# Performance work log

Hardware: AMD Instinct MI355X
Metric: run time of the kernel (lower is better)

The kernel has to match this reference:

```python
import jax, jax.numpy as jnp
import numpy as np

DIM = 1024
HEADS = 16
DIM_HEAD = 64
INNER = HEADS * DIM_HEAD  # 1024
SCALE = DIM_HEAD ** -0.5


def setup_inputs() -> dict:
    key = jax.random.key(0)
    k0, k1, k2 = jax.random.split(key, 3)
    x = jax.random.normal(k0, (4, 2048, DIM), dtype=jnp.float32)
    ln_gamma = jnp.ones((DIM,), dtype=jnp.float32)
    ln_beta = jnp.zeros((DIM,), dtype=jnp.float32)
    w_qkv = jax.random.normal(k1, (DIM, 3 * INNER), dtype=jnp.float32) * (DIM ** -0.5)
    w_out = jax.random.normal(k2, (INNER, DIM), dtype=jnp.float32) * (INNER ** -0.5)
    b_out = jnp.zeros((DIM,), dtype=jnp.float32)
    return {"x": x, "ln_gamma": ln_gamma, "ln_beta": ln_beta,
            "w_qkv": w_qkv, "w_out": w_out, "b_out": b_out}


def reference(x, ln_gamma, ln_beta, w_qkv, w_out, b_out):
    # LayerNorm over last dim (eps matches torch default 1e-5)
    mu = jnp.mean(x, axis=-1, keepdims=True)
    var = jnp.mean(jnp.square(x - mu), axis=-1, keepdims=True)
    xn = (x - mu) * jax.lax.rsqrt(var + 1e-5) * ln_gamma + ln_beta
    # QKV projection (no bias)
    qkv = xn @ w_qkv  # [b, t, 3*inner]
    q, k, v = jnp.split(qkv, 3, axis=-1)
    B, T, _ = x.shape
    def to_heads(t):
        return t.reshape(B, T, HEADS, DIM_HEAD).transpose(0, 2, 1, 3)  # b h t d
    q, k, v = to_heads(q), to_heads(k), to_heads(v)
    dots = jnp.einsum('bhid,bhjd->bhij', q, k) * SCALE
    attn = jax.nn.softmax(dots, axis=-1)
    out = jnp.einsum('bhij,bhjd->bhid', attn, v)
    out = out.transpose(0, 2, 1, 3).reshape(B, T, INNER)
    return out @ w_out + b_out
```

## Files before the change

### kernel.cpp

```cpp
#include <hip/hip_runtime.h>


#define DIMX 1024
#define TSEQ 2048
#define NB 4
#define NH 16
#define DH 64
#define NROWS (NB * TSEQ)
#define QSCALE 0.18033688011112042f

typedef __bf16 bf16_t;
typedef __bf16 bf16x8 __attribute__((ext_vector_type(8)));
typedef __bf16 bf16x4 __attribute__((ext_vector_type(4)));
typedef float f32x4 __attribute__((ext_vector_type(4)));

#if __has_builtin(__builtin_amdgcn_exp2f)
#define EXP2F __builtin_amdgcn_exp2f
#else
#define EXP2F exp2f
#endif

__device__ __forceinline__ bf16x4 cvt4(f32x4 v) {
    return __builtin_convertvector(v, bf16x4);
}
__device__ __forceinline__ void async16(const bf16_t* g, bf16_t* l) {
    __builtin_amdgcn_global_load_lds(
        (const __attribute__((address_space(1))) unsigned int*)g,
        (__attribute__((address_space(3))) unsigned int*)l, 16, 0, 0);
}

__global__ __launch_bounds__(256) void prep_kernel(
    const float* __restrict__ x, const float* __restrict__ g,
    const float* __restrict__ b, bf16_t* __restrict__ xn,
    const float* __restrict__ w_qkv, bf16_t* __restrict__ wqkvT,
    const float* __restrict__ w_out, bf16_t* __restrict__ woutT) {
    int bid = blockIdx.x, tid = threadIdx.x;
    if (bid < NROWS) {
        int row = bid;
        const float4 xv = *(const float4*)(x + (size_t)row * DIMX + tid * 4);
        float s = xv.x + xv.y + xv.z + xv.w;
        float q = xv.x * xv.x + xv.y * xv.y + xv.z * xv.z + xv.w * xv.w;
        for (int o = 32; o > 0; o >>= 1) {
            s += __shfl_xor(s, o);
            q += __shfl_xor(q, o);
        }
        __shared__ float2 red[4];
        int wave = tid >> 6, lane = tid & 63;
        if (lane == 0) red[wave] = make_float2(s, q);
        __syncthreads();
        float2 r0 = red[0], r1 = red[1], r2 = red[2], r3 = red[3];
        s = r0.x + r1.x + r2.x + r3.x;
        q = r0.y + r1.y + r2.y + r3.y;
        float mu = s * (1.0f / DIMX);
        float var = q * (1.0f / DIMX) - mu * mu;
        float rstd = rsqrtf(var + 1e-5f);
        float4 gv = *(const float4*)(g + tid * 4);
        float4 bv = *(const float4*)(b + tid * 4);
        f32x4 r;
        r[0] = (xv.x - mu) * rstd * gv.x + bv.x;
        r[1] = (xv.y - mu) * rstd * gv.y + bv.y;
        r[2] = (xv.z - mu) * rstd * gv.z + bv.z;
        r[3] = (xv.w - mu) * rstd * gv.w + bv.w;
        *(bf16x4*)(xn + (size_t)row * DIMX + tid * 4) = cvt4(r);
    } else {
        const float* src;
        bf16_t* dst;
        int R, C, tb;
        if (bid < NROWS + 3072) {
            tb = bid - NROWS; src = w_qkv; dst = wqkvT; R = 1024; C = 3072;
        } else {
            tb = bid - NROWS - 3072; src = w_out; dst = woutT; R = 1024; C = 1024;
        }
        int ntx = C >> 5;
        int c0 = (tb % ntx) * 32, r0 = (tb / ntx) * 32;
        int tx = tid & 31, ty = tid >> 5;
        __shared__ float tile[32][33];
        for (int i = ty; i < 32; i += 8)
            tile[i][tx] = src[(size_t)(r0 + i) * C + c0 + tx];
        __syncthreads();
        for (int i = ty; i < 32; i += 8)
            dst[(size_t)(c0 + i) * R + r0 + tx] = (bf16_t)tile[tx][i];
    }
}

#define MFMA16 __builtin_amdgcn_mfma_f32_16x16x32_bf16

template <int MODE>
__device__ __forceinline__ void gemm_epilogue(
    f32x4 (&acc)[4][4], void* Cout, const float* bias,
    int m0, int n0, int wr, int wc, int lm, int quad, int N) {
#pragma unroll
    for (int mt = 0; mt < 4; ++mt) {
#pragma unroll
        for (int nt = 0; nt < 4; ++nt) {
            int m = m0 + wr * 64 + mt * 16 + quad * 4;
            int n = n0 + wc * 64 + nt * 16 + lm;
            if (MODE == 1) {
                int sel = n >> 10, nn = n & 1023, h = nn >> 6, d = nn & 63;
                int b = m >> 11, t = m & 2047;
                if (sel == 2) {
                    *(bf16x4*)((bf16_t*)Cout + (size_t)2 * 8388608 +
                               ((size_t)((b * NH + h) * DH + d)) * TSEQ + t) = cvt4(acc[mt][nt]);
                } else {
                    f32x4 sv = acc[mt][nt] * (sel == 0 ? QSCALE : 1.0f);
                    bf16x4 c4 = cvt4(sv);
#pragma unroll
                    for (int r = 0; r < 4; ++r)
                        ((bf16_t*)Cout)[(size_t)sel * 8388608 +
                                        ((size_t)((b * NH + h) * TSEQ + t + r)) * DH + d] = c4[r];
                }
            } else {
                float bn = bias[n];
#pragma unroll
                for (int r = 0; r < 4; ++r)
                    ((float*)Cout)[(size_t)(m + r) * N + n] = acc[mt][nt][r] + bn;
            }
        }
    }
}

template <int MODE>
__global__ __launch_bounds__(256, 2) void gemm128p(
    const bf16_t* __restrict__ A, const bf16_t* __restrict__ BT,
    void* __restrict__ Cout, const float* __restrict__ bias, int M, int N, int K) {
    __shared__ __align__(16) bf16_t As[2][128 * 64];
    __shared__ __align__(16) bf16_t Bs[2][128 * 64];
    int tid = threadIdx.x, lane = tid & 63, wave = tid >> 6;
    int lm = lane & 15, quad = lane >> 4;
    int wr = wave >> 1, wc = wave & 1;

    int nbx = gridDim.x;
    int nwg = nbx * gridDim.y;
    int linear = blockIdx.y * nbx + blockIdx.x;
    int cpx = nwg >> 3;
    int swz = (linear & 7) * cpx + (linear >> 3);
    int bx = swz % nbx, by = swz / nbx;
    int m0 = by * 128, n0 = bx * 128;

    int srow = tid >> 3, sc8 = tid & 7;
    int scol = (sc8 ^ (srow & 7)) << 3;
    const bf16_t* ga = A + (size_t)(m0 + srow) * K + scol;
    const bf16_t* gb = BT + (size_t)(n0 + srow) * K + scol;
    int ldst = tid << 3;

    int sw0 = ((quad ^ (lm & 7)) << 3);
    int sw1 = (((4 + quad) ^ (lm & 7)) << 3);

    f32x4 zero = {0.f, 0.f, 0.f, 0.f};
    f32x4 acc[4][4];
#pragma unroll
    for (int i = 0; i < 4; ++i)
#pragma unroll
        for (int j = 0; j < 4; ++j) acc[i][j] = zero;

#pragma unroll
    for (int i = 0; i < 4; ++i) async16(ga + (size_t)(i * 32) * K, &As[0][i * 2048 + ldst]);
#pragma unroll
    for (int i = 0; i < 4; ++i) async16(gb + (size_t)(i * 32) * K, &Bs[0][i * 2048 + ldst]);
    asm volatile("s_waitcnt vmcnt(0)" ::: "memory");
    __builtin_amdgcn_s_barrier();

    int nkt = K >> 6;
    for (int kt = 0; kt < nkt; ++kt) {
        int c = kt & 1;
        int k1 = (kt + 1) << 6;
        bool pf = (kt + 1) < nkt;
        const bf16_t* pa = &As[c][0];
        const bf16_t* pb = &Bs[c][0];
        bf16_t* na = &As[c ^ 1][0];
        bf16_t* nb = &Bs[c ^ 1][0];
        bf16x8 af[4][2], bfr[2][2];

#pragma unroll
        for (int t = 0; t < 4; ++t) {
            int ro = (wr * 64 + t * 16 + lm) * 64;
            af[t][0] = *(const bf16x8*)&pa[ro + sw0];
            af[t][1] = *(const bf16x8*)&pa[ro + sw1];
        }
#pragma unroll
        for (int t = 0; t < 2; ++t) {
            int ro = (wc * 64 + t * 16 + lm) * 64;
            bfr[t][0] = *(const bf16x8*)&pb[ro + sw0];
            bfr[t][1] = *(const bf16x8*)&pb[ro + sw1];
        }
        if (pf) {
#pragma unroll
            for (int i = 0; i < 4; ++i)
                async16(ga + (size_t)(i * 32) * K + k1, &na[i * 2048 + ldst]);
#pragma unroll
            for (int i = 0; i < 4; ++i)
                async16(gb + (size_t)(i * 32) * K + k1, &nb[i * 2048 + ldst]);
        }
        __builtin_amdgcn_s_barrier();
        asm volatile("s_waitcnt lgkmcnt(0)" ::: "memory");
        __builtin_amdgcn_s_setprio(1);
#pragma unroll
        for (int mt = 0; mt < 4; ++mt)
#pragma unroll
            for (int nt = 0; nt < 2; ++nt) {
                acc[mt][nt] = MFMA16(af[mt][0], bfr[nt][0], acc[mt][nt], 0, 0, 0);
                acc[mt][nt] = MFMA16(af[mt][1], bfr[nt][1], acc[mt][nt], 0, 0, 0);
            }
        __builtin_amdgcn_s_setprio(0);
        __builtin_amdgcn_s_barrier();

#pragma unroll
        for (int t = 0; t < 2; ++t) {
            int ro = (wc * 64 + (2 + t) * 16 + lm) * 64;
            bfr[t][0] = *(const bf16x8*)&pb[ro + sw0];
            bfr[t][1] = *(const bf16x8*)&pb[ro + sw1];
        }
        __builtin_amdgcn_s_barrier();
        asm volatile("s_waitcnt lgkmcnt(0)" ::: "memory");
        __builtin_amdgcn_s_setprio(1);
#pragma unroll
        for (int mt = 0; mt < 4; ++mt)
#pragma unroll
            for (int nt = 0; nt < 2; ++nt) {
                acc[mt][2 + nt] = MFMA16(af[mt][0], bfr[nt][0], acc[mt][2 + nt], 0, 0, 0);
                acc[mt][2 + nt] = MFMA16(af[mt][1], bfr[nt][1], acc[mt][2 + nt], 0, 0, 0);
            }
        __builtin_amdgcn_s_setprio(0);
        asm volatile("s_waitcnt vmcnt(0)" ::: "memory");
        __builtin_amdgcn_s_barrier();
    }

    gemm_epilogue<MODE>(acc, Cout, bias, m0, n0, wr, wc, lm, quad, N);
}

__global__ __launch_bounds__(512, 4) void attn_mfma(
    const bf16_t* __restrict__ qkv, bf16_t* __restrict__ o) {
    int bh = blockIdx.y;
    int qt = blockIdx.x;
    const bf16_t* qb = qkv + (size_t)bh * TSEQ * DH;
    const bf16_t* kb = qkv + (size_t)8388608 + (size_t)bh * TSEQ * DH;
    const bf16_t* vb = qkv + (size_t)16777216 + (size_t)bh * DH * TSEQ;
    int tid = threadIdx.x, wave = tid >> 6, lane = tid & 63;
    int lm = lane & 15, quad = lane >> 4, lx = lm & 7;

    __shared__ __align__(16) bf16_t Ks[2][2][64 * 64];
    __shared__ __align__(16) bf16_t Vt[2][2][64 * 64];

    int roff = tid >> 3;
    int fr = (roff & 3) | ((roff & 8) >> 1);
    int cperm = ((tid & 7) ^ fr) * 8;
    const bf16_t* kp = kb + (size_t)roff * DH + cperm;
    const bf16_t* vp = vb + (size_t)roff * TSEQ + cperm;
    int l0 = tid * 8;

    bf16x8 qf[2][2];
#pragma unroll
    for (int u = 0; u < 2; ++u)
#pragma unroll
        for (int ks = 0; ks < 2; ++ks)
            qf[u][ks] = *(const bf16x8*)(qb +
                (size_t)(qt * 256 + wave * 32 + u * 16 + lm) * DH + ks * 32 + quad * 8);

    f32x4 zero = {0.f, 0.f, 0.f, 0.f};
    f32x4 m16 = {-16.f, -16.f, -16.f, -16.f};
    f32x4 acc[2][4];
#pragma unroll
    for (int u = 0; u < 2; ++u)
#pragma unroll
        for (int dt = 0; dt < 4; ++dt) acc[u][dt] = zero;
    f32x4 l4[2] = {zero, zero};

    int qh = lm >> 2, rr = lm & 3;
    int krow0 = 8 * qh + rr;
    int krow1 = krow0 + 4;
    int krow2 = 32 + 8 * (qh ^ 2) + rr;
    int krow3 = krow2 + 4;
    int fo0 = (quad ^ lx) * 8;
    int fo1 = ((4 + quad) ^ lx) * 8;
    int fv = (lm & 3) | ((lm & 8) >> 1);
    int vo0 = (quad ^ fv) * 8;
    int vo1 = ((4 | (quad ^ 2)) ^ fv) * 8;

    async16(kp, &Ks[0][0][l0]);
    async16(kp + (size_t)64 * DH, &Ks[0][1][l0]);
    async16(vp, &Vt[0][0][l0]);
    async16(vp + 64, &Vt[0][1][l0]);
    kp += 128 * DH; vp += 128;
    asm volatile("s_waitcnt vmcnt(0)" ::: "memory");
    __builtin_amdgcn_s_barrier();

    for (int jt = 0; jt < TSEQ / 128; ++jt) {
        int c = jt & 1;
        if (jt + 1 < TSEQ / 128) {
            async16(kp, &Ks[c ^ 1][0][l0]);
            async16(kp + (size_t)64 * DH, &Ks[c ^ 1][1][l0]);
            async16(vp, &Vt[c ^ 1][0][l0]);
            async16(vp + 64, &Vt[c ^ 1][1][l0]);
            kp += 128 * DH; vp += 128;
        }

#pragma unroll
        for (int sub = 0; sub < 2; ++sub) {
            const bf16_t* Kc = &Ks[c][sub][0];
            const bf16_t* Vc = &Vt[c][sub][0];

            bf16x8 kf[4][2];
            kf[0][0] = *(const bf16x8*)&Kc[krow0 * 64 + fo0];
            kf[0][1] = *(const bf16x8*)&Kc[krow0 * 64 + fo1];
            kf[1][0] = *(const bf16x8*)&Kc[krow1 * 64 + fo0];
            kf[1][1] = *(const bf16x8*)&Kc[krow1 * 64 + fo1];
            kf[2][0] = *(const bf16x8*)&Kc[krow2 * 64 + fo0];
            kf[2][1] = *(const bf16x8*)&Kc[krow2 * 64 + fo1];
            kf[3][0] = *(const bf16x8*)&Kc[krow3 * 64 + fo0];
            kf[3][1] = *(const bf16x8*)&Kc[krow3 * 64 + fo1];

            f32x4 s2[2][4];
            __builtin_amdgcn_s_setprio(1);
#pragma unroll
            for (int u = 0; u < 2; ++u)
#pragma unroll
                for (int nt = 0; nt < 4; ++nt) {
                    s2[u][nt] = __builtin_amdgcn_mfma_f32_16x16x32_bf16(kf[nt][0], qf[u][0], m16, 0, 0, 0);
                    s2[u][nt] = __builtin_amdgcn_mfma_f32_16x16x32_bf16(kf[nt][1], qf[u][1], s2[u][nt], 0, 0, 0);
                }
            __builtin_amdgcn_s_setprio(0);

            bf16x8 pf[2][2];
#pragma unroll
            for (int u = 0; u < 2; ++u) {
                f32x4 p[4];
#pragma unroll
                for (int nt = 0; nt < 4; ++nt) {
#pragma unroll
                    for (int e = 0; e < 4; ++e) p[nt][e] = EXP2F(s2[u][nt][e]);
                    l4[u] += p[nt];
                }
                bf16x4 c0 = cvt4(p[0]), c1 = cvt4(p[1]), c2 = cvt4(p[2]), c3 = cvt4(p[3]);
                pf[u][0] = __builtin_shufflevector(c0, c1, 0, 1, 2, 3, 4, 5, 6, 7);
                pf[u][1] = __builtin_shufflevector(c2, c3, 0, 1, 2, 3, 4, 5, 6, 7);
            }

            __builtin_amdgcn_s_setprio(1);
#pragma unroll
            for (int dt = 0; dt < 4; ++dt) {
                bf16x8 vf0 = *(const bf16x8*)&Vc[(dt * 16 + lm) * 64 + vo0];
                bf16x8 vf1 = *(const bf16x8*)&Vc[(dt * 16 + lm) * 64 + vo1];
#pragma unroll
                for (int u = 0; u < 2; ++u) {
                    acc[u][dt] = __builtin_amdgcn_mfma_f32_16x16x32_bf16(vf0, pf[u][0], acc[u][dt], 0, 0, 0);
                    acc[u][dt] = __builtin_amdgcn_mfma_f32_16x16x32_bf16(vf1, pf[u][1], acc[u][dt], 0, 0, 0);
                }
            }
            __builtin_amdgcn_s_setprio(0);
        }

        asm volatile("s_waitcnt vmcnt(0)" ::: "memory");
        __builtin_amdgcn_s_barrier();
    }

    int b = bh >> 4, h = bh & 15;
#pragma unroll
    for (int u = 0; u < 2; ++u) {
        float l = (l4[u][0] + l4[u][1]) + (l4[u][2] + l4[u][3]);
        l += __shfl_xor(l, 16);
        l += __shfl_xor(l, 32);
        float rl = 1.0f / l;
        int t = qt * 256 + wave * 32 + u * 16 + lm;
#pragma unroll
        for (int dt = 0; dt < 4; ++dt) {
            f32x4 ov = acc[u][dt] * rl;
            *(bf16x4*)(o + ((size_t)(b * TSEQ + t)) * DIMX + h * DH + dt * 16 + quad * 4) = cvt4(ov);
        }
    }
}

extern "C" void kernel_launch(void* const* d_in, const int* in_sizes, int n_in,
                              void* d_out, int out_size, void* d_ws, size_t ws_size,
                              hipStream_t stream) {
    const float* x = (const float*)d_in[0];
    const float* g = (const float*)d_in[1];
    const float* be = (const float*)d_in[2];
    const float* w_qkv = (const float*)d_in[3];
    const float* w_out = (const float*)d_in[4];
    const float* b_out = (const float*)d_in[5];
    float* out = (float*)d_out;
    char* ws = (char*)d_ws;

    bf16_t* xn = (bf16_t*)(ws);
    bf16_t* wqkvT = (bf16_t*)(ws + 16777216);
    bf16_t* woutT = (bf16_t*)(ws + 23068672);
    bf16_t* qkv = (bf16_t*)(ws + 25165824);
    bf16_t* attno = (bf16_t*)(ws + 75497472);

    prep_kernel<<<NROWS + 3072 + 1024, 256, 0, stream>>>(
        x, g, be, xn, w_qkv, wqkvT, w_out, woutT);
    gemm128p<1><<<dim3(24, 64), 256, 0, stream>>>(xn, wqkvT, (void*)qkv, nullptr, NROWS, 3072, 1024);
    attn_mfma<<<dim3(8, 64), 512, 0, stream>>>(qkv, attno);
    gemm128p<2><<<dim3(8, 64), 256, 0, stream>>>(attno, woutT, (void*)out, b_out, NROWS, 1024, 1024);
}
```

Before: 258.4 us.

## Use 256x256-tile 8-wave GEMM kernel for QKV projection

Adds a new GEMM kernel with 256x256 output tiles, 512 threads and 8 waves, each wave computing a 128x64 sub-tile. A and B halves are staged asynchronously into double-buffered LDS, and the loads are interleaved with four MFMA phases per K-step. The larger tile is meant to cut global and LDS traffic per FLOP for the QKV projection. In exchange it uses more registers and 128KB of LDS, limiting occupancy to one block per CU, and the grid shrinks to 384 blocks, which may leave the 256 CUs unevenly loaded.

```diff
diff --git a/kernel.cpp b/kernel.cpp
--- a/kernel.cpp
+++ b/kernel.cpp
@@ -86,37 +86,190 @@
 #define MFMA16 __builtin_amdgcn_mfma_f32_16x16x32_bf16
 
 template <int MODE>
-__device__ __forceinline__ void gemm_epilogue(
-    f32x4 (&acc)[4][4], void* Cout, const float* bias,
-    int m0, int n0, int wr, int wc, int lm, int quad, int N) {
-#pragma unroll
-    for (int mt = 0; mt < 4; ++mt) {
+__device__ __forceinline__ void cwrite_frag(
+    f32x4 v, void* Cout, const float* bias, int m, int n, int N) {
+    if (MODE == 1) {
+        int sel = n >> 10, nn = n & 1023, h = nn >> 6, d = nn & 63;
+        int b = m >> 11, t = m & 2047;
+        if (sel == 2) {
+            *(bf16x4*)((bf16_t*)Cout + (size_t)2 * 8388608 +
+                       ((size_t)((b * NH + h) * DH + d)) * TSEQ + t) = cvt4(v);
+        } else {
+            f32x4 sv = v * (sel == 0 ? QSCALE : 1.0f);
+            bf16x4 c4 = cvt4(sv);
+#pragma unroll
+            for (int r = 0; r < 4; ++r)
+                ((bf16_t*)Cout)[(size_t)sel * 8388608 +
+                                ((size_t)((b * NH + h) * TSEQ + t + r)) * DH + d] = c4[r];
+        }
+    } else {
+        float bn = bias[n];
+#pragma unroll
+        for (int r = 0; r < 4; ++r)
+            ((float*)Cout)[(size_t)(m + r) * N + n] = v[r] + bn;
+    }
+}
+
+template <int MODE>
+__global__ __launch_bounds__(512, 1) void gemm256t(
+    const bf16_t* __restrict__ A, const bf16_t* __restrict__ BT,
+    void* __restrict__ Cout, const float* __restrict__ bias, int M, int N, int K) {
+    __shared__ __align__(16) bf16_t Ah[2][2][128 * 64];
+    __shared__ __align__(16) bf16_t Bh[2][2][128 * 64];
+    int tid = threadIdx.x, lane = tid & 63, wave = tid >> 6;
+    int lm = lane & 15, quad = lane >> 4;
+    int wr = wave >> 2, wc = wave & 3;
+
+    int nbx = gridDim.x;
+    int nwg = nbx * gridDim.y;
+    int linear = blockIdx.y * nbx + blockIdx.x;
+    int cpx = nwg >> 3;
+    int swz = (linear & 7) * cpx + (linear >> 3);
+    int bx = swz % nbx, by = swz / nbx;
+    int m0 = by * 256, n0 = bx * 256;
+
+    int srow = tid >> 3;
+    int scol = ((tid & 7) ^ (srow & 7)) << 3;
+    const bf16_t* ga = A + (size_t)(m0 + srow) * K + scol;
+    const bf16_t* gb = BT + (size_t)(n0 + srow) * K + scol;
+    int ldst = tid * 8;
+
+#define STAGE_A(t, H)                                                          \
+    do {                                                                       \
+        size_t k0 = (size_t)(t) << 6;                                          \
+        async16(ga + (size_t)((H) * 128) * K + k0, &Ah[(t)&1][H][ldst]);       \
+        async16(ga + (size_t)((H) * 128 + 64) * K + k0,                        \
+                &Ah[(t)&1][H][4096 + ldst]);                                   \
+    } while (0)
+#define STAGE_B(t, H)                                                          \
+    do {                                                                       \
+        size_t k0 = (size_t)(t) << 6;                                          \
+        async16(gb + (size_t)((H) * 128) * K + k0, &Bh[(t)&1][H][ldst]);       \
+        async16(gb + (size_t)((H) * 128 + 64) * K + k0,                        \
+                &Bh[(t)&1][H][4096 + ldst]);                                   \
+    } while (0)
+
+    int sw0 = ((quad ^ (lm & 7)) << 3);
+    int sw1 = (((4 + quad) ^ (lm & 7)) << 3);
+    int brow = (wc & 1) * 64;
+
+    f32x4 zero = {0.f, 0.f, 0.f, 0.f};
+    f32x4 acc[8][4];
+#pragma unroll
+    for (int i = 0; i < 8; ++i)
+#pragma unroll
+        for (int j = 0; j < 4; ++j) acc[i][j] = zero;
+
+    STAGE_A(0, 0);
+    STAGE_A(0, 1);
+    STAGE_B(0, 0);
+    STAGE_B(0, 1);
+    STAGE_A(1, 0);
+    STAGE_A(1, 1);
+
+    int nkt = K >> 6;
+    bf16x8 af[4][2], bfa[2][2], bfb[2][2];
+    for (int t = 0; t < nkt; ++t) {
+        int s = t & 1;
+        const bf16_t* pA = &Ah[s][wr][0];
+        const bf16_t* pB = &Bh[s][wc >> 1][0];
+
+        if (t + 1 < nkt) STAGE_B(t + 1, 0);
+        if (t < nkt - 1)
+            asm volatile("s_waitcnt vmcnt(6)" ::: "memory");
+        else
+            asm volatile("s_waitcnt vmcnt(0)" ::: "memory");
+        __builtin_amdgcn_s_barrier();
+#pragma unroll
+        for (int mt = 0; mt < 4; ++mt) {
+            int ro = (mt * 16 + lm) * 64;
+            af[mt][0] = *(const bf16x8*)&pA[ro + sw0];
+            af[mt][1] = *(const bf16x8*)&pA[ro + sw1];
+        }
+#pragma unroll
+        for (int nt = 0; nt < 2; ++nt) {
+            int ro = (brow + nt * 16 + lm) * 64;
+            bfa[nt][0] = *(const bf16x8*)&pB[ro + sw0];
+            bfa[nt][1] = *(const bf16x8*)&pB[ro + sw1];
+        }
+        asm volatile("s_waitcnt lgkmcnt(0)" ::: "memory");
+        __builtin_amdgcn_s_setprio(1);
+#pragma unroll
+        for (int mt = 0; mt < 4; ++mt)
+#pragma unroll
+            for (int nt = 0; nt < 2; ++nt) {
+                acc[mt][nt] = MFMA16(af[mt][0], bfa[nt][0], acc[mt][nt], 0, 0, 0);
+                acc[mt][nt] = MFMA16(af[mt][1], bfa[nt][1], acc[mt][nt], 0, 0, 0);
+            }
+        __builtin_amdgcn_s_setprio(0);
+        __builtin_amdgcn_s_barrier();
+
+#pragma unroll
+        for (int nt = 0; nt < 2; ++nt) {
+            int ro = (brow + (2 + nt) * 16 + lm) * 64;
+            bfb[nt][0] = *(const bf16x8*)&pB[ro + sw0];
+            bfb[nt][1] = *(const bf16x8*)&pB[ro + sw1];
+        }
+        if (t + 1 < nkt) STAGE_B(t + 1, 1);
+        __builtin_amdgcn_s_barrier();
+        asm volatile("s_waitcnt lgkmcnt(0)" ::: "memory");
+        __builtin_amdgcn_s_setprio(1);
+#pragma unroll
+        for (int mt = 0; mt < 4; ++mt)
+#pragma unroll
+            for (int nt = 0; nt < 2; ++nt) {
+                acc[mt][2 + nt] = MFMA16(af[mt][0], bfb[nt][0], acc[mt][2 + nt], 0, 0, 0);
+                acc[mt][2 + nt] = MFMA16(af[mt][1], bfb[nt][1], acc[mt][2 + nt], 0, 0, 0);
+            }
+        __builtin_amdgcn_s_setprio(0);
+        __builtin_amdgcn_s_barrier();
+
+#pragma unroll
+        for (int mt = 0; mt < 4; ++mt) {
+            int ro = (64 + mt * 16 + lm) * 64;
+            af[mt][0] = *(const bf16x8*)&pA[ro + sw0];
+            af[mt][1] = *(const bf16x8*)&pA[ro + sw1];
+        }
+        __builtin_amdgcn_s_barrier();
+        asm volatile("s_waitcnt lgkmcnt(0)" ::: "memory");
+        __builtin_amdgcn_s_setprio(1);
+#pragma unroll
+        for (int mt = 0; mt < 4; ++mt)
+#pragma unroll
+            for (int nt = 0; nt < 2; ++nt) {
+                acc[4 + mt][2 + nt] = MFMA16(af[mt][0], bfb[nt][0], acc[4 + mt][2 + nt], 0, 0, 0);
+                acc[4 + mt][2 + nt] = MFMA16(af[mt][1], bfb[nt][1], acc[4 + mt][2 + nt], 0, 0, 0);
+            }
+        __builtin_amdgcn_s_setprio(0);
+        __builtin_amdgcn_s_barrier();
+
+        if (t + 2 < nkt) {
+            STAGE_A(t + 2, 0);
+            STAGE_A(t + 2, 1);
+        }
+        __builtin_amdgcn_s_barrier();
+        __builtin_amdgcn_s_setprio(1);
+#pragma unroll
+        for (int mt = 0; mt < 4; ++mt)
+#pragma unroll
+            for (int nt = 0; nt < 2; ++nt) {
+                acc[4 + mt][nt] = MFMA16(af[mt][0], bfa[nt][0], acc[4 + mt][nt], 0, 0, 0);
+                acc[4 + mt][nt] = MFMA16(af[mt][1], bfa[nt][1], acc[4 + mt][nt], 0, 0, 0);
+            }
+        __builtin_amdgcn_s_setprio(0);
+        __builtin_amdgcn_s_barrier();
+    }
+#undef STAGE_A
+#undef STAGE_B
+
+#pragma unroll
+    for (int mt = 0; mt < 8; ++mt)
 #pragma unroll
         for (int nt = 0; nt < 4; ++nt) {
-            int m = m0 + wr * 64 + mt * 16 + quad * 4;
+            int m = m0 + wr * 128 + mt * 16 + quad * 4;
             int n = n0 + wc * 64 + nt * 16 + lm;
-            if (MODE == 1) {
-                int sel = n >> 10, nn = n & 1023, h = nn >> 6, d = nn & 63;
-                int b = m >> 11, t = m & 2047;
-                if (sel == 2) {
-                    *(bf16x4*)((bf16_t*)Cout + (size_t)2 * 8388608 +
-                               ((size_t)((b * NH + h) * DH + d)) * TSEQ + t) = cvt4(acc[mt][nt]);
-                } else {
-                    f32x4 sv = acc[mt][nt] * (sel == 0 ? QSCALE : 1.0f);
-                    bf16x4 c4 = cvt4(sv);
-#pragma unroll
-                    for (int r = 0; r < 4; ++r)
-                        ((bf16_t*)Cout)[(size_t)sel * 8388608 +
-                                        ((size_t)((b * NH + h) * TSEQ + t + r)) * DH + d] = c4[r];
-                }
-            } else {
-                float bn = bias[n];
-#pragma unroll
-                for (int r = 0; r < 4; ++r)
-                    ((float*)Cout)[(size_t)(m + r) * N + n] = acc[mt][nt][r] + bn;
-            }
-        }
-    }
+            cwrite_frag<MODE>(acc[mt][nt], Cout, bias, m, n, N);
+        }
 }
 
 template <int MODE>
@@ -225,7 +378,14 @@
         __builtin_amdgcn_s_barrier();
     }
 
-    gemm_epilogue<MODE>(acc, Cout, bias, m0, n0, wr, wc, lm, quad, N);
+#pragma unroll
+    for (int mt = 0; mt < 4; ++mt)
+#pragma unroll
+        for (int nt = 0; nt < 4; ++nt) {
+            int m = m0 + wr * 64 + mt * 16 + quad * 4;
+            int n = n0 + wc * 64 + nt * 16 + lm;
+            cwrite_frag<MODE>(acc[mt][nt], Cout, bias, m, n, N);
+        }
 }
 
 __global__ __launch_bounds__(512, 4) void attn_mfma(
@@ -389,7 +549,7 @@
 
     prep_kernel<<<NROWS + 3072 + 1024, 256, 0, stream>>>(
         x, g, be, xn, w_qkv, wqkvT, w_out, woutT);
-    gemm128p<1><<<dim3(24, 64), 256, 0, stream>>>(xn, wqkvT, (void*)qkv, nullptr, NROWS, 3072, 1024);
+    gemm256t<1><<<dim3(12, 32), 512, 0, stream>>>(xn, wqkvT, (void*)qkv, nullptr, NROWS, 3072, 1024);
     attn_mfma<<<dim3(8, 64), 512, 0, stream>>>(qkv, attno);
     gemm128p<2><<<dim3(8, 64), 256, 0, stream>>>(attno, woutT, (void*)out, b_out, NROWS, 1024, 1024);
 }
```

Measured after the change: 272.8 us. 1.06x slower.
